# Performance work log

Measured on AMD Instinct MI355X. Metric: run time of the kernel, lower is better.

The kernel has to match this reference:

```python
import jax, jax.numpy as jnp
import numpy as np

B, Q, CTX, H, HKV, D, HID = 2, 1024, 3072, 32, 8, 128, 4096
KV = CTX + Q
EPS = 1e-6


def _rope_tables():
    pos = jnp.arange(KV, dtype=jnp.float32)
    inv_freq = 1.0 / (10000.0 ** (jnp.arange(0, D, 2, dtype=jnp.float32) / D))
    ang = pos[:, None] * inv_freq[None, :]              # [KV, D/2]
    emb = jnp.concatenate([ang, ang], axis=-1)          # [KV, D]
    cos = jnp.broadcast_to(jnp.cos(emb)[None], (B, KV, D))
    sin = jnp.broadcast_to(jnp.sin(emb)[None], (B, KV, D))
    return cos, sin


def setup_inputs() -> dict:
    key = jax.random.key(0)
    ks = jax.random.split(key, 8)
    cos, sin = _rope_tables()
    return {
        "hidden_states": jax.random.normal(ks[0], (B, Q, HID), jnp.float32),
        "context_states": jax.random.normal(ks[1], (B, CTX, HID), jnp.float32),
        "cos": cos,
        "sin": sin,
        "attention_mask": jnp.zeros((B, 1, Q, KV), jnp.float32),
        "Wq": jax.random.normal(ks[2], (HID, H * D), jnp.float32) * 0.02,
        "Wk": jax.random.normal(ks[3], (HID, HKV * D), jnp.float32) * 0.02,
        "Wv": jax.random.normal(ks[4], (HID, HKV * D), jnp.float32) * 0.02,
        "Wo": jax.random.normal(ks[5], (H * D, HID), jnp.float32) * 0.02,
        "q_norm_w": jnp.ones((D,), jnp.float32),
        "k_norm_w": jnp.ones((D,), jnp.float32),
    }


def _rms_norm(x, w):
    var = jnp.mean(x * x, axis=-1, keepdims=True)
    return x * jax.lax.rsqrt(var + EPS) * w


def _rotate_half(x):
    x1, x2 = jnp.split(x, 2, axis=-1)
    return jnp.concatenate([-x2, x1], axis=-1)


def reference(hidden_states, context_states, cos, sin, attention_mask,
              Wq, Wk, Wv, Wo, q_norm_w, k_norm_w):
    # q projection + per-head RMSNorm
    q = (hidden_states @ Wq).reshape(B, Q, H, D)
    q = _rms_norm(q, q_norm_w).transpose(0, 2, 1, 3)      # [B,H,Q,D]
    # k/v: context tokens then noise tokens
    k = jnp.concatenate([context_states @ Wk, hidden_states @ Wk], axis=1)
    k = _rms_norm(k.reshape(B, KV, HKV, D), k_norm_w).transpose(0, 2, 1, 3)  # [B,Hkv,KV,D]
    v = jnp.concatenate([context_states @ Wv, hidden_states @ Wv], axis=1)
    v = v.reshape(B, KV, HKV, D).transpose(0, 2, 1, 3)    # [B,Hkv,KV,D]
    # rotary: q takes the trailing q_len positions of the kv-length tables
    cos4 = cos[:, None, :, :]                             # [B,1,KV,D]
    sin4 = sin[:, None, :, :]
    q = q * cos4[..., -Q:, :] + _rotate_half(q) * sin4[..., -Q:, :]
    k = k * cos4 + _rotate_half(k) * sin4
    # GQA: repeat kv heads to match query heads
    g = H // HKV
    kr = jnp.repeat(k, g, axis=1)                         # [B,H,KV,D]
    vr = jnp.repeat(v, g, axis=1)
    scale = D ** -0.5
    scores = jnp.einsum("bhqd,bhkd->bhqk", q, kr) * scale + attention_mask
    attn = jax.nn.softmax(scores, axis=-1)
    out = jnp.einsum("bhqk,bhkd->bhqd", attn, vr)         # [B,H,Q,D]
    out = out.transpose(0, 2, 1, 3).reshape(B, Q, H * D)
    return out @ Wo
```

## Files before the change

kernel.cpp:

```cpp
#include <hip/hip_runtime.h>
#include <stdint.h>

typedef unsigned short u16;
typedef __attribute__((ext_vector_type(4))) float f32x4;
typedef __attribute__((ext_vector_type(8))) __bf16 bf16x8;
typedef __attribute__((ext_vector_type(2))) __bf16 bf16x2;

#define B_   2
#define Q_   1024
#define CTX_ 3072
#define KV_  4096
#define H_   32
#define HKV_ 8
#define D_   128
#define HID_ 4096

__device__ __forceinline__ u16 f2bf(float f) {
  uint32_t u = __float_as_uint(f);
  u += 0x7fffu + ((u >> 16) & 1u);
  return (u16)(u >> 16);
}
__device__ __forceinline__ float bf2f(u16 h) {
  return __uint_as_float(((uint32_t)h) << 16);
}
__device__ __forceinline__ uint32_t packbf2(float a, float b) {
  return (uint32_t)f2bf(a) | ((uint32_t)f2bf(b) << 16);
}
__device__ __forceinline__ uint32_t pkbf(float a, float b) {
  bf16x2 v = {(__bf16)a, (__bf16)b};
  uint32_t r;
  __builtin_memcpy(&r, &v, 4);
  return r;
}
__device__ __forceinline__ float fexp2(float x) {
#if __has_builtin(__builtin_amdgcn_exp2f)
  return __builtin_amdgcn_exp2f(x);
#else
  return exp2f(x);
#endif
}
__device__ __forceinline__ f32x4 zero4() { f32x4 v = {0.f, 0.f, 0.f, 0.f}; return v; }

__device__ __forceinline__ f32x4 mfma16(bf16x8 a, bf16x8 b, f32x4 c) {
  return __builtin_amdgcn_mfma_f32_16x16x32_bf16(a, b, c, 0, 0, 0);
}

__device__ __forceinline__ void gl2lds16(const void* g, void* l) {
  __builtin_amdgcn_global_load_lds(
      (const __attribute__((address_space(1))) void*)g,
      (__attribute__((address_space(3))) void*)l, 16, 0, 0);
}

__device__ __forceinline__ void bar()    { asm volatile("s_barrier" ::: "memory"); }
__device__ __forceinline__ void waitv8() { asm volatile("s_waitcnt vmcnt(8)" ::: "memory"); }
__device__ __forceinline__ void waitv0() { asm volatile("s_waitcnt vmcnt(0)" ::: "memory"); }

__global__ void conv_bf16(const float* __restrict__ in, u16* __restrict__ out, int n8) {
  int i = blockIdx.x * blockDim.x + threadIdx.x;
  if (i >= n8) return;
  const float4 a = *reinterpret_cast<const float4*>(in + (size_t)i * 8);
  const float4 b = *reinterpret_cast<const float4*>(in + (size_t)i * 8 + 4);
  uint4 o;
  o.x = packbf2(a.x, a.y); o.y = packbf2(a.z, a.w);
  o.z = packbf2(b.x, b.y); o.w = packbf2(b.z, b.w);
  *reinterpret_cast<uint4*>(out + (size_t)i * 8) = o;
}

__global__ void transpose_w(const float* __restrict__ W, u16* __restrict__ WT, int K, int N) {
  __shared__ u16 t[64][68];
  const int n0 = blockIdx.x * 64, k0 = blockIdx.y * 64;
  const int tid = threadIdx.x;
  const int rr = tid >> 4;
  const int cc = (tid & 15) * 4;
#pragma unroll
  for (int p = 0; p < 4; ++p) {
    const int r = p * 16 + rr;
    const float4 v = *reinterpret_cast<const float4*>(W + (size_t)(k0 + r) * N + n0 + cc);
    t[cc + 0][r] = f2bf(v.x);
    t[cc + 1][r] = f2bf(v.y);
    t[cc + 2][r] = f2bf(v.z);
    t[cc + 3][r] = f2bf(v.w);
  }
  __syncthreads();
#pragma unroll
  for (int p = 0; p < 4; ++p) {
    const int n = p * 16 + rr;
    const uint2 w = *reinterpret_cast<const uint2*>(&t[n][cc]);
    *reinterpret_cast<uint2*>(WT + (size_t)(n0 + n) * K + k0 + cc) = w;
  }
}

template <int MODE>
__global__ __launch_bounds__(256, 2) void gemm_bt(
    const u16* __restrict__ A0, const u16* __restrict__ A1,
    const u16* __restrict__ B0, const u16* __restrict__ B1,
    void* __restrict__ Cv, int N) {
  __shared__ u16 lA[2][128 * 64];
  __shared__ u16 lB[2][128 * 64];
  const int tid = threadIdx.x;
  const int lane = tid & 63, wid = tid >> 6;
  const int lq = lane & 15, lg = lane >> 4;
  const int nbn = N >> 7;
  const int bm = (int)blockIdx.x / nbn, bn = (int)blockIdx.x % nbn;
  const int m0 = bm << 7, n0 = bn << 7;
  const int wr = wid >> 1, wc = wid & 1;
  const int sr = lane >> 3;
  const int sc = (lane & 7) << 4;

  f32x4 acc[4][4];
#pragma unroll
  for (int i = 0; i < 4; ++i)
#pragma unroll
    for (int j = 0; j < 4; ++j) acc[i][j] = zero4();

  auto arowp = [&](int m) -> const u16* {
    if constexpr (MODE == 1) {
      const int b = m >> 12, kv = m & 4095;
      return (kv < CTX_) ? (A0 + (size_t)(b * CTX_ + kv) * HID_)
                         : (A1 + (size_t)(b * Q_ + (kv - CTX_)) * HID_);
    } else {
      return A0 + (size_t)m * HID_;
    }
  };
  auto browp = [&](int n) -> const u16* {
    if constexpr (MODE == 1) {
      return (n < 1024) ? (B0 + (size_t)n * HID_) : (B1 + (size_t)(n - 1024) * HID_);
    } else {
      return B0 + (size_t)n * HID_;
    }
  };

  const char* apre[4];
  const char* bpre[4];
#pragma unroll
  for (int j = 0; j < 4; ++j) {
    const int r0 = (wid * 4 + j) * 8;
    const int r = r0 + sr;
    const int sw = sc ^ ((r & 7) << 4);
    apre[j] = (const char*)arowp(m0 + r) + sw;
    bpre[j] = (const char*)browp(n0 + r) + sw;
  }

  auto stage = [&](int cur, int kt) {
    const int kb = kt << 7;
#pragma unroll
    for (int j = 0; j < 4; ++j) {
      const int r0 = (wid * 4 + j) * 8;
      gl2lds16(apre[j] + kb, (char*)&lA[cur][0] + r0 * 128);
      gl2lds16(bpre[j] + kb, (char*)&lB[cur][0] + r0 * 128);
    }
  };

  const int NK = HID_ / 64;
  stage(0, 0);
  stage(1, 1);
  waitv8();
  bar();

  for (int kt = 0; kt < NK; ++kt) {
    const int cur = kt & 1;
    const char* ba = (const char*)&lA[cur][0];
    const char* bb = (const char*)&lB[cur][0];
    bf16x8 af[4][2], bfr[4][2];
#pragma unroll
    for (int mf = 0; mf < 4; ++mf)
#pragma unroll
      for (int kk = 0; kk < 2; ++kk)
        af[mf][kk] = *reinterpret_cast<const bf16x8*>(
            ba + (wr * 64 + mf * 16 + lq) * 128 + ((kk * 64 + lg * 16) ^ ((lq & 7) << 4)));
#pragma unroll
    for (int nf = 0; nf < 4; ++nf)
#pragma unroll
      for (int kk = 0; kk < 2; ++kk)
        bfr[nf][kk] = *reinterpret_cast<const bf16x8*>(
            bb + (wc * 64 + nf * 16 + lq) * 128 + ((kk * 64 + lg * 16) ^ ((lq & 7) << 4)));
    __builtin_amdgcn_s_setprio(1);
#pragma unroll
    for (int mf = 0; mf < 4; ++mf)
#pragma unroll
      for (int nf = 0; nf < 4; ++nf) {
        acc[mf][nf] = mfma16(af[mf][0], bfr[nf][0], acc[mf][nf]);
        acc[mf][nf] = mfma16(af[mf][1], bfr[nf][1], acc[mf][nf]);
      }
    __builtin_amdgcn_s_setprio(0);
    bar();
    if (kt + 2 < NK) {
      stage(cur, kt + 2);
      waitv8();
      bar();
    } else if (kt + 1 < NK) {
      waitv0();
      bar();
    }
  }

#pragma unroll
  for (int mf = 0; mf < 4; ++mf) {
    const int m = m0 + wr * 64 + mf * 16 + lg * 4;
#pragma unroll
    for (int nf = 0; nf < 4; ++nf) {
      const int n = n0 + wc * 64 + nf * 16 + lq;
      if constexpr (MODE == 2) {
        float* C = (float*)Cv;
#pragma unroll
        for (int i = 0; i < 4; ++i) C[(size_t)(m + i) * N + n] = acc[mf][nf][i];
      } else {
        u16* C = (u16*)Cv;
#pragma unroll
        for (int i = 0; i < 4; ++i) C[(size_t)(m + i) * N + n] = f2bf(acc[mf][nf][i]);
      }
    }
  }
}

__global__ void rope_q(const u16* __restrict__ Qp, const float* __restrict__ cosT,
                       const float* __restrict__ sinT, const float* __restrict__ w,
                       u16* __restrict__ Qh) {
  const int row = blockIdx.x * 4 + (threadIdx.x >> 6);
  const int lane = threadIdx.x & 63;
  const int b = row >> 15;
  const int rem = row & 32767;
  const int q = rem >> 5, h = rem & 31;
  const int d = lane * 2;
  const uint32_t raw =
      *reinterpret_cast<const uint32_t*>(Qp + (size_t)(b * Q_ + q) * HID_ + h * D_ + d);
  float x0 = bf2f((u16)(raw & 0xffffu)), x1 = bf2f((u16)(raw >> 16));
  float ss = x0 * x0 + x1 * x1;
#pragma unroll
  for (int m = 1; m < 64; m <<= 1) ss += __shfl_xor(ss, m);
  const float rms = rsqrtf(ss * (1.0f / 128.0f) + 1e-6f);
  const float n0v = x0 * rms * w[d], n1v = x1 * rms * w[d + 1];
  const float p0 = __shfl_xor(n0v, 32), p1 = __shfl_xor(n1v, 32);
  const float r0 = (lane < 32) ? -p0 : p0;
  const float r1 = (lane < 32) ? -p1 : p1;
  const int pos = CTX_ + q;
  const size_t cb = (size_t)(b * KV_ + pos) * D_ + d;
  const float y0 = n0v * cosT[cb] + r0 * sinT[cb];
  const float y1 = n1v * cosT[cb + 1] + r1 * sinT[cb + 1];
  *reinterpret_cast<uint32_t*>(Qh + (size_t)((b * H_ + h) * Q_ + q) * D_ + d) = packbf2(y0, y1);
}

__global__ void rope_k(const u16* __restrict__ KVp, const float* __restrict__ cosT,
                       const float* __restrict__ sinT, const float* __restrict__ w,
                       u16* __restrict__ Kt) {
  const int row = blockIdx.x * 4 + (threadIdx.x >> 6);
  const int lane = threadIdx.x & 63;
  const int b = row >> 15;
  const int rem = row & 32767;
  const int kv = rem >> 3, hk = rem & 7;
  const int d = lane * 2;
  const uint32_t raw =
      *reinterpret_cast<const uint32_t*>(KVp + (size_t)(b * KV_ + kv) * 2048 + hk * D_ + d);
  float x0 = bf2f((u16)(raw & 0xffffu)), x1 = bf2f((u16)(raw >> 16));
  float ss = x0 * x0 + x1 * x1;
#pragma unroll
  for (int m = 1; m < 64; m <<= 1) ss += __shfl_xor(ss, m);
  const float rms = rsqrtf(ss * (1.0f / 128.0f) + 1e-6f);
  const float n0v = x0 * rms * w[d], n1v = x1 * rms * w[d + 1];
  const float p0 = __shfl_xor(n0v, 32), p1 = __shfl_xor(n1v, 32);
  const float r0 = (lane < 32) ? -p0 : p0;
  const float r1 = (lane < 32) ? -p1 : p1;
  const size_t cb = (size_t)(b * KV_ + kv) * D_ + d;
  const float y0 = n0v * cosT[cb] + r0 * sinT[cb];
  const float y1 = n1v * cosT[cb + 1] + r1 * sinT[cb + 1];
  *reinterpret_cast<uint32_t*>(Kt + ((size_t)(b * HKV_ + hk) * KV_ + kv) * D_ + d) =
      packbf2(y0, y1);
}

__global__ void transpose_v(const u16* __restrict__ KVp, u16* __restrict__ Vt) {
  __shared__ u16 t[128][68];
  const int bid = (int)blockIdx.x;
  const int kt = bid & 63;
  const int rest = bid >> 6;
  const int hk = rest & 7, b = rest >> 3;
  const int kv0 = kt * 64;
  const int tid = threadIdx.x;
  const int kvi = tid >> 5;
  const int d4 = (tid & 31) * 4;
#pragma unroll
  for (int p = 0; p < 8; ++p) {
    const int kv = p * 8 + kvi;
    const uint2 v = *reinterpret_cast<const uint2*>(
        KVp + (size_t)(b * KV_ + kv0 + kv) * 2048 + 1024 + hk * D_ + d4);
    t[d4 + 0][kv] = (u16)(v.x & 0xffffu);
    t[d4 + 1][kv] = (u16)(v.x >> 16);
    t[d4 + 2][kv] = (u16)(v.y & 0xffffu);
    t[d4 + 3][kv] = (u16)(v.y >> 16);
  }
  __syncthreads();
  const int dr = tid >> 4;
  const int k4 = (tid & 15) * 4;
#pragma unroll
  for (int p = 0; p < 8; ++p) {
    const int dd = p * 16 + dr;
    const uint2 w = *reinterpret_cast<const uint2*>(&t[dd][k4]);
    *reinterpret_cast<uint2*>(Vt + ((size_t)(b * HKV_ + hk) * D_ + dd) * KV_ + kv0 + k4) = w;
  }
}

__global__ __launch_bounds__(256, 2) void attn(
    const u16* __restrict__ Qh, const u16* __restrict__ Kt,
    const u16* __restrict__ Vt, u16* __restrict__ O) {
  __shared__ u16 lK[2][64 * 128];
  __shared__ u16 lV[2][128 * 64];
  __shared__ u16 lP[4][2][16 * 64];
  const int bid0 = (int)blockIdx.x;
  const int lb = (bid0 & 7) * 64 + (bid0 >> 3);
  const int qt = lb & 7;
  const int rest = lb >> 3;
  const int g4 = rest & 3;
  const int bhk = rest >> 2;
  const int b = bhk >> 3, hk = bhk & 7;
  const int h = hk * 4 + g4;
  const int tid = threadIdx.x;
  const int lane = tid & 63, wid = tid >> 6;
  const int lq = lane & 15, lg = lane >> 4;
  const int q0 = qt * 128 + wid * 32;

  const char* qrow = (const char*)(Qh + ((size_t)(b * H_ + h) * Q_ + q0 + lq) * D_);
  bf16x8 qf[2][4];
#pragma unroll
  for (int kk = 0; kk < 4; ++kk) {
    qf[0][kk] = *reinterpret_cast<const bf16x8*>(qrow + kk * 64 + lg * 16);
    qf[1][kk] = *reinterpret_cast<const bf16x8*>(qrow + 16 * 256 + kk * 64 + lg * 16);
  }

  const char* KtB = (const char*)(Kt + (size_t)(b * HKV_ + hk) * KV_ * D_);
  const char* VtB = (const char*)(Vt + (size_t)(b * HKV_ + hk) * D_ * KV_);

  f32x4 oac[2][8];
#pragma unroll
  for (int qb = 0; qb < 2; ++qb)
#pragma unroll
    for (int i = 0; i < 8; ++i) oac[qb][i] = zero4();
  float mrow[2] = {-1e30f, -1e30f}, lsum[2] = {0.f, 0.f};

  const int kr = lane >> 4;
  const int kcb = (lane & 15) << 4;
  const int vr = lane >> 3;
  const int vcb = (lane & 7) << 4;

  const char* kpre[4];
  const char* vpre[4];
#pragma unroll
  for (int j = 0; j < 4; ++j) {
    const int krow = (wid * 4 + j) * 4 + kr;
    kpre[j] = KtB + (size_t)krow * 256 + (kcb ^ ((krow & 7) << 4));
    const int dd = (wid * 4 + j) * 8 + vr;
    vpre[j] = VtB + (size_t)dd * (KV_ * 2) + (vcb ^ ((dd & 7) << 4));
  }

  auto stage = [&](int cur, int t) {
    const size_t kv0 = (size_t)(t << 6);
#pragma unroll
    for (int j = 0; j < 4; ++j) {
      const int r0 = (wid * 4 + j) * 4;
      gl2lds16(kpre[j] + kv0 * 256, (char*)&lK[cur][0] + r0 * 256);
    }
#pragma unroll
    for (int j = 0; j < 4; ++j) {
      const int d0 = (wid * 4 + j) * 8;
      gl2lds16(vpre[j] + kv0 * 2, (char*)&lV[cur][0] + d0 * 128);
    }
  };

  const int NT = KV_ / 64;
  stage(0, 0);
  stage(1, 1);
  waitv8();
  bar();

  const float c1 = 0.12752134f;
  char* pb0 = (char*)&lP[wid][0][0];
  char* pb1 = (char*)&lP[wid][1][0];
  for (int t = 0; t < NT; ++t) {
    const int cur = t & 1;
    const char* kb = (const char*)&lK[cur][0];
    const char* vb = (const char*)&lV[cur][0];
    f32x4 sa[2][4];
    __builtin_amdgcn_s_setprio(1);
#pragma unroll
    for (int h16 = 0; h16 < 4; ++h16) {
      const int row = h16 * 16 + lq;
      bf16x8 kf[4];
#pragma unroll
      for (int kk = 0; kk < 4; ++kk)
        kf[kk] = *reinterpret_cast<const bf16x8*>(
            kb + row * 256 + ((kk * 64 + lg * 16) ^ ((lq & 7) << 4)));
      f32x4 s0 = zero4(), s1 = zero4();
#pragma unroll
      for (int kk = 0; kk < 4; ++kk) {
        s0 = mfma16(kf[kk], qf[0][kk], s0);
        s1 = mfma16(kf[kk], qf[1][kk], s1);
      }
      sa[0][h16] = s0;
      sa[1][h16] = s1;
    }
    __builtin_amdgcn_s_setprio(0);
#pragma unroll
    for (int qb = 0; qb < 2; ++qb) {
      const f32x4 s0v = sa[qb][0], s1v = sa[qb][1], s2v = sa[qb][2], s3v = sa[qb][3];
      float ta = fmaxf(fmaxf(s0v[0], s0v[1]), s0v[2]);
      float tb = fmaxf(fmaxf(s0v[3], s1v[0]), s1v[1]);
      float tc = fmaxf(fmaxf(s1v[2], s1v[3]), s2v[0]);
      float td = fmaxf(fmaxf(s2v[1], s2v[2]), s2v[3]);
      float te = fmaxf(fmaxf(s3v[0], s3v[1]), s3v[2]);
      float tmax = fmaxf(fmaxf(fmaxf(ta, tb), tc), fmaxf(fmaxf(td, te), s3v[3]));
      tmax = fmaxf(tmax, __shfl_xor(tmax, 16));
      tmax = fmaxf(tmax, __shfl_xor(tmax, 32));
      float p[4][4];
      if (!__all((tmax - mrow[qb]) * c1 <= 3.0f)) {
        const float mnew = fmaxf(mrow[qb], tmax);
        const float resc = fexp2((mrow[qb] - mnew) * c1);
        mrow[qb] = mnew;
        lsum[qb] *= resc;
#pragma unroll
        for (int i = 0; i < 8; ++i) oac[qb][i] *= resc;
      }
      const float mc = mrow[qb] * c1;
#pragma unroll
      for (int h16 = 0; h16 < 4; ++h16)
#pragma unroll
        for (int i = 0; i < 4; ++i)
          p[h16][i] = fexp2(fmaf(sa[qb][h16][i], c1, -mc));
      float q01 = (p[0][0] + p[0][1]) + (p[0][2] + p[0][3]);
      float q23 = (p[1][0] + p[1][1]) + (p[1][2] + p[1][3]);
      float q45 = (p[2][0] + p[2][1]) + (p[2][2] + p[2][3]);
      float q67 = (p[3][0] + p[3][1]) + (p[3][2] + p[3][3]);
      lsum[qb] += (q01 + q23) + (q45 + q67);
      char* pb = qb ? pb1 : pb0;
#pragma unroll
      for (int h16 = 0; h16 < 4; ++h16) {
        uint2 pw;
        pw.x = pkbf(p[h16][0], p[h16][1]);
        pw.y = pkbf(p[h16][2], p[h16][3]);
        *reinterpret_cast<uint2*>(pb + lq * 128 + ((h16 * 32 + lg * 8) ^ ((lq & 7) << 4))) = pw;
      }
    }
    asm volatile("" ::: "memory");
    __builtin_amdgcn_s_setprio(1);
#pragma unroll
    for (int c = 0; c < 2; ++c) {
      const int po = lq * 128 + ((lg * 16 + c * 64) ^ ((lq & 7) << 4));
      const bf16x8 pf0 = *reinterpret_cast<const bf16x8*>(pb0 + po);
      const bf16x8 pf1 = *reinterpret_cast<const bf16x8*>(pb1 + po);
#pragma unroll
      for (int db = 0; db < 8; ++db) {
        const int dd = db * 16 + lq;
        const bf16x8 vf = *reinterpret_cast<const bf16x8*>(
            vb + dd * 128 + ((lg * 16 + c * 64) ^ ((dd & 7) << 4)));
        oac[0][db] = mfma16(vf, pf0, oac[0][db]);
        oac[1][db] = mfma16(vf, pf1, oac[1][db]);
      }
    }
    __builtin_amdgcn_s_setprio(0);
    bar();
    if (t + 2 < NT) {
      stage(cur, t + 2);
      waitv8();
      bar();
    } else if (t + 1 < NT) {
      waitv0();
      bar();
    }
  }
#pragma unroll
  for (int qb = 0; qb < 2; ++qb) {
    float lt = lsum[qb] + __shfl_xor(lsum[qb], 16);
    lt += __shfl_xor(lt, 32);
    const float inv = 1.0f / lt;
    u16* orow = O + (size_t)(b * Q_ + q0 + qb * 16 + lq) * (H_ * D_) + h * D_;
#pragma unroll
    for (int db = 0; db < 8; ++db) {
      uint2 wv;
      wv.x = pkbf(oac[qb][db][0] * inv, oac[qb][db][1] * inv);
      wv.y = pkbf(oac[qb][db][2] * inv, oac[qb][db][3] * inv);
      *reinterpret_cast<uint2*>((char*)orow + db * 32 + lg * 8) = wv;
    }
  }
}

extern "C" void kernel_launch(void* const* d_in, const int* in_sizes, int n_in,
                              void* d_out, int out_size, void* d_ws, size_t ws_size,
                              hipStream_t stream) {
  (void)in_sizes; (void)n_in; (void)out_size; (void)ws_size;
  const float* hidden  = (const float*)d_in[0];
  const float* context = (const float*)d_in[1];
  const float* cosT    = (const float*)d_in[2];
  const float* sinT    = (const float*)d_in[3];
  const float* Wq = (const float*)d_in[5];
  const float* Wk = (const float*)d_in[6];
  const float* Wv = (const float*)d_in[7];
  const float* Wo = (const float*)d_in[8];
  const float* qw = (const float*)d_in[9];
  const float* kw = (const float*)d_in[10];

  char* ws = (char*)d_ws;
  u16* hidB = (u16*)(ws + 0);
  u16* ctxB = (u16*)(ws + 16777216);
  u16* WqT  = (u16*)(ws + 67108864);
  u16* WkT  = (u16*)(ws + 100663296);
  u16* WvT  = (u16*)(ws + 109051904);
  u16* WoT  = (u16*)(ws + 117440512);
  u16* Qp   = (u16*)(ws + 150994944);
  u16* KVp  = (u16*)(ws + 167772160);
  u16* Qh   = (u16*)(ws + 201326592);
  u16* Kt   = (u16*)(ws + 218103808);
  u16* Vt   = (u16*)(ws + 234881024);
  u16* Obuf = hidB;

  conv_bf16<<<4096, 256, 0, stream>>>(hidden, hidB, 1048576);
  conv_bf16<<<12288, 256, 0, stream>>>(context, ctxB, 3145728);
  transpose_w<<<dim3(64, 64), 256, 0, stream>>>(Wq, WqT, 4096, 4096);
  transpose_w<<<dim3(16, 64), 256, 0, stream>>>(Wk, WkT, 4096, 1024);
  transpose_w<<<dim3(16, 64), 256, 0, stream>>>(Wv, WvT, 4096, 1024);
  transpose_w<<<dim3(64, 64), 256, 0, stream>>>(Wo, WoT, 4096, 4096);
  gemm_bt<0><<<512, 256, 0, stream>>>(hidB, nullptr, WqT, nullptr, Qp, 4096);
  gemm_bt<1><<<1024, 256, 0, stream>>>(ctxB, hidB, WkT, WvT, KVp, 2048);
  rope_q<<<16384, 256, 0, stream>>>(Qp, cosT, sinT, qw, Qh);
  rope_k<<<16384, 256, 0, stream>>>(KVp, cosT, sinT, kw, Kt);
  transpose_v<<<1024, 256, 0, stream>>>(KVp, Vt);
  attn<<<512, 256, 0, stream>>>(Qh, Kt, Vt, Obuf);
  gemm_bt<2><<<512, 256, 0, stream>>>(Obuf, nullptr, WoT, nullptr, d_out, 4096);
}
```

Measured before the change: 618.1 us.

## Use dedicated 256x256-tile 8-wave GEMM for fused K/V projection

Replaces the 128x128-tile generic GEMM for the K/V projection with a new kernel that uses 256x256 tiles, 512 threads and a split-K-half staging schedule. Loads are interleaved with MFMA phases, wave priority is raised around the MFMA blocks, and the block index is remapped to group tiles for L2 reuse. The aim is more operand reuse per byte loaded and better overlap of global-to-LDS traffic with compute. The cost is higher register pressure from the 8x4 accumulators and more barriers per K step. The generic GEMM drops its unused dual-pointer mode.

```diff
diff --git a/kernel.cpp b/kernel.cpp
--- a/kernel.cpp
+++ b/kernel.cpp
@@ -53,6 +53,7 @@
 
 __device__ __forceinline__ void bar()    { asm volatile("s_barrier" ::: "memory"); }
 __device__ __forceinline__ void waitv8() { asm volatile("s_waitcnt vmcnt(8)" ::: "memory"); }
+__device__ __forceinline__ void waitv4() { asm volatile("s_waitcnt vmcnt(4)" ::: "memory"); }
 __device__ __forceinline__ void waitv0() { asm volatile("s_waitcnt vmcnt(0)" ::: "memory"); }
 
 __global__ void conv_bf16(const float* __restrict__ in, u16* __restrict__ out, int n8) {
@@ -92,8 +93,7 @@
 
 template <int MODE>
 __global__ __launch_bounds__(256, 2) void gemm_bt(
-    const u16* __restrict__ A0, const u16* __restrict__ A1,
-    const u16* __restrict__ B0, const u16* __restrict__ B1,
+    const u16* __restrict__ A0, const u16* __restrict__ B0,
     void* __restrict__ Cv, int N) {
   __shared__ u16 lA[2][128 * 64];
   __shared__ u16 lB[2][128 * 64];
@@ -113,23 +113,6 @@
 #pragma unroll
     for (int j = 0; j < 4; ++j) acc[i][j] = zero4();
 
-  auto arowp = [&](int m) -> const u16* {
-    if constexpr (MODE == 1) {
-      const int b = m >> 12, kv = m & 4095;
-      return (kv < CTX_) ? (A0 + (size_t)(b * CTX_ + kv) * HID_)
-                         : (A1 + (size_t)(b * Q_ + (kv - CTX_)) * HID_);
-    } else {
-      return A0 + (size_t)m * HID_;
-    }
-  };
-  auto browp = [&](int n) -> const u16* {
-    if constexpr (MODE == 1) {
-      return (n < 1024) ? (B0 + (size_t)n * HID_) : (B1 + (size_t)(n - 1024) * HID_);
-    } else {
-      return B0 + (size_t)n * HID_;
-    }
-  };
-
   const char* apre[4];
   const char* bpre[4];
 #pragma unroll
@@ -137,8 +120,8 @@
     const int r0 = (wid * 4 + j) * 8;
     const int r = r0 + sr;
     const int sw = sc ^ ((r & 7) << 4);
-    apre[j] = (const char*)arowp(m0 + r) + sw;
-    bpre[j] = (const char*)browp(n0 + r) + sw;
+    apre[j] = (const char*)(A0 + (size_t)(m0 + r) * HID_) + sw;
+    bpre[j] = (const char*)(B0 + (size_t)(n0 + r) * HID_) + sw;
   }
 
   auto stage = [&](int cur, int kt) {
@@ -209,6 +192,142 @@
 #pragma unroll
         for (int i = 0; i < 4; ++i) C[(size_t)(m + i) * N + n] = f2bf(acc[mf][nf][i]);
       }
+    }
+  }
+}
+
+__global__ __launch_bounds__(512, 2) void gemm_kv8(
+    const u16* __restrict__ A0, const u16* __restrict__ A1,
+    const u16* __restrict__ B0, const u16* __restrict__ B1,
+    u16* __restrict__ C) {
+  __shared__ u16 lA[2][2][256 * 32];
+  __shared__ u16 lB[2][2][256 * 32];
+  const int tid = threadIdx.x;
+  const int lane = tid & 63, wid = tid >> 6;
+  const int lq = lane & 15, lg = lane >> 4;
+  const int lb = ((int)blockIdx.x & 7) * 32 + ((int)blockIdx.x >> 3);
+  const int bm = lb >> 3, bn = lb & 7;
+  const int m0 = bm << 8, n0 = bn << 8;
+  const int wr = wid >> 2, wc = wid & 3;
+
+  f32x4 acc[8][4];
+#pragma unroll
+  for (int i = 0; i < 8; ++i)
+#pragma unroll
+    for (int j = 0; j < 4; ++j) acc[i][j] = zero4();
+
+  auto arowp = [&](int m) -> const u16* {
+    const int b = m >> 12, kv = m & 4095;
+    return (kv < CTX_) ? (A0 + (size_t)(b * CTX_ + kv) * HID_)
+                       : (A1 + (size_t)(b * Q_ + (kv - CTX_)) * HID_);
+  };
+  auto browp = [&](int n) -> const u16* {
+    return (n < 1024) ? (B0 + (size_t)n * HID_) : (B1 + (size_t)(n - 1024) * HID_);
+  };
+
+  const char* apre[2];
+  const char* bpre[2];
+  int ldst[2];
+#pragma unroll
+  for (int j = 0; j < 2; ++j) {
+    const int rr = wid * 32 + j * 16 + (lane >> 2);
+    const int ch = ((lane & 3) ^ ((rr >> 1) & 3)) << 4;
+    apre[j] = (const char*)arowp(m0 + rr) + ch;
+    bpre[j] = (const char*)browp(n0 + rr) + ch;
+    ldst[j] = (wid * 32 + j * 16) * 64;
+  }
+
+  auto stageA = [&](int buf, int kh, int t) {
+    const int kb = (t << 7) + (kh << 6);
+#pragma unroll
+    for (int j = 0; j < 2; ++j)
+      gl2lds16(apre[j] + kb, (char*)&lA[buf][kh][0] + ldst[j]);
+  };
+  auto stageB = [&](int buf, int kh, int t) {
+    const int kb = (t << 7) + (kh << 6);
+#pragma unroll
+    for (int j = 0; j < 2; ++j)
+      gl2lds16(bpre[j] + kb, (char*)&lB[buf][kh][0] + ldst[j]);
+  };
+
+  auto rdA = [&](int buf, int kh, int mf) -> bf16x8 {
+    const int row = wr * 128 + mf * 16 + lq;
+    return *reinterpret_cast<const bf16x8*>(
+        (const char*)&lA[buf][kh][0] + row * 64 + ((lg * 16) ^ (((row >> 1) & 3) << 4)));
+  };
+  auto rdB = [&](int buf, int kh, int nf) -> bf16x8 {
+    const int row = wc * 64 + nf * 16 + lq;
+    return *reinterpret_cast<const bf16x8*>(
+        (const char*)&lB[buf][kh][0] + row * 64 + ((lg * 16) ^ (((row >> 1) & 3) << 4)));
+  };
+
+  const int NK = HID_ / 64;
+  stageA(0, 0, 0); stageB(0, 0, 0); stageA(0, 1, 0); stageB(0, 1, 0);
+
+  bf16x8 af[4], bfr[4];
+  for (int t = 0; t < NK; ++t) {
+    const int buf = t & 1, nb = buf ^ 1;
+    const bool pf = (t + 1 < NK);
+    waitv4();
+    if (pf) stageA(nb, 0, t + 1);
+    bar();
+#pragma unroll
+    for (int mf = 0; mf < 4; ++mf) af[mf] = rdA(buf, 0, mf);
+#pragma unroll
+    for (int nf = 0; nf < 4; ++nf) bfr[nf] = rdB(buf, 0, nf);
+    __builtin_amdgcn_s_setprio(1);
+#pragma unroll
+    for (int mf = 0; mf < 4; ++mf)
+#pragma unroll
+      for (int nf = 0; nf < 4; ++nf) acc[mf][nf] = mfma16(af[mf], bfr[nf], acc[mf][nf]);
+    __builtin_amdgcn_s_setprio(0);
+    bar();
+    if (pf) stageB(nb, 0, t + 1);
+    bar();
+#pragma unroll
+    for (int mf = 0; mf < 4; ++mf) af[mf] = rdA(buf, 0, mf + 4);
+    __builtin_amdgcn_s_setprio(1);
+#pragma unroll
+    for (int mf = 0; mf < 4; ++mf)
+#pragma unroll
+      for (int nf = 0; nf < 4; ++nf) acc[mf + 4][nf] = mfma16(af[mf], bfr[nf], acc[mf + 4][nf]);
+    __builtin_amdgcn_s_setprio(0);
+    bar();
+    if (pf) { waitv4(); stageA(nb, 1, t + 1); }
+    else    { waitv0(); }
+    bar();
+#pragma unroll
+    for (int mf = 0; mf < 4; ++mf) af[mf] = rdA(buf, 1, mf);
+#pragma unroll
+    for (int nf = 0; nf < 4; ++nf) bfr[nf] = rdB(buf, 1, nf);
+    __builtin_amdgcn_s_setprio(1);
+#pragma unroll
+    for (int mf = 0; mf < 4; ++mf)
+#pragma unroll
+      for (int nf = 0; nf < 4; ++nf) acc[mf][nf] = mfma16(af[mf], bfr[nf], acc[mf][nf]);
+    __builtin_amdgcn_s_setprio(0);
+    bar();
+    if (pf) stageB(nb, 1, t + 1);
+    bar();
+#pragma unroll
+    for (int mf = 0; mf < 4; ++mf) af[mf] = rdA(buf, 1, mf + 4);
+    __builtin_amdgcn_s_setprio(1);
+#pragma unroll
+    for (int mf = 0; mf < 4; ++mf)
+#pragma unroll
+      for (int nf = 0; nf < 4; ++nf) acc[mf + 4][nf] = mfma16(af[mf], bfr[nf], acc[mf + 4][nf]);
+    __builtin_amdgcn_s_setprio(0);
+    bar();
+  }
+
+#pragma unroll
+  for (int mf = 0; mf < 8; ++mf) {
+    const int m = m0 + wr * 128 + mf * 16 + lg * 4;
+#pragma unroll
+    for (int nf = 0; nf < 4; ++nf) {
+      const int n = n0 + wc * 64 + nf * 16 + lq;
+#pragma unroll
+      for (int i = 0; i < 4; ++i) C[(size_t)(m + i) * 2048 + n] = f2bf(acc[mf][nf][i]);
     }
   }
 }
@@ -515,11 +634,11 @@
   transpose_w<<<dim3(16, 64), 256, 0, stream>>>(Wk, WkT, 4096, 1024);
   transpose_w<<<dim3(16, 64), 256, 0, stream>>>(Wv, WvT, 4096, 1024);
   transpose_w<<<dim3(64, 64), 256, 0, stream>>>(Wo, WoT, 4096, 4096);
-  gemm_bt<0><<<512, 256, 0, stream>>>(hidB, nullptr, WqT, nullptr, Qp, 4096);
-  gemm_bt<1><<<1024, 256, 0, stream>>>(ctxB, hidB, WkT, WvT, KVp, 2048);
+  gemm_bt<0><<<512, 256, 0, stream>>>(hidB, WqT, Qp, 4096);
+  gemm_kv8<<<256, 512, 0, stream>>>(ctxB, hidB, WkT, WvT, KVp);
   rope_q<<<16384, 256, 0, stream>>>(Qp, cosT, sinT, qw, Qh);
   rope_k<<<16384, 256, 0, stream>>>(KVp, cosT, sinT, kw, Kt);
   transpose_v<<<1024, 256, 0, stream>>>(KVp, Vt);
   attn<<<512, 256, 0, stream>>>(Qh, Kt, Vt, Obuf);
-  gemm_bt<2><<<512, 256, 0, stream>>>(Obuf, nullptr, WoT, nullptr, d_out, 4096);
-}
+  gemm_bt<2><<<512, 256, 0, stream>>>(Obuf, WoT, d_out, 4096);
+}
```

New measurement: 623.9 us. No clear change (+0.9%).

## Fuse RMSNorm+RoPE and V transpose into projection GEMM epilogues

Applied to the files above, without the earlier changes.

The Q and K/V projection GEMMs now stage their fp32 accumulators in shared memory and apply per-head RMSNorm and rotary embedding (or transpose V) directly in the epilogue. This removes three separate elementwise/transpose kernels and the intermediate Qp/KVp round trip through global memory. LDS offsets in the GEMM and attention loops are also precomputed once into registers. Shared memory grows to 128x129 floats per block (about 66 KB), which may lower occupancy. The epilogue also adds a serial per-thread pass over 64 elements with cos/sin loads.

```diff
diff --git a/kernel.cpp b/kernel.cpp
--- a/kernel.cpp
+++ b/kernel.cpp
@@ -91,12 +91,15 @@
 }
 
 template <int MODE>
-__global__ __launch_bounds__(256, 2) void gemm_bt(
+__global__ __launch_bounds__(256, 2) void gemm_fused(
     const u16* __restrict__ A0, const u16* __restrict__ A1,
     const u16* __restrict__ B0, const u16* __restrict__ B1,
-    void* __restrict__ Cv, int N) {
-  __shared__ u16 lA[2][128 * 64];
-  __shared__ u16 lB[2][128 * 64];
+    const float* __restrict__ cosT, const float* __restrict__ sinT,
+    const float* __restrict__ nw,
+    void* __restrict__ out0, void* __restrict__ out1, int N) {
+  __shared__ float scr[128 * 129];
+  u16* lA = (u16*)scr;
+  u16* lB = lA + 2 * 128 * 64;
   const int tid = threadIdx.x;
   const int lane = tid & 63, wid = tid >> 6;
   const int lq = lane & 15, lg = lane >> 4;
@@ -141,13 +144,22 @@
     bpre[j] = (const char*)browp(n0 + r) + sw;
   }
 
+  int aoff[4][2], boff[4][2];
+#pragma unroll
+  for (int mf = 0; mf < 4; ++mf)
+#pragma unroll
+    for (int kk = 0; kk < 2; ++kk) {
+      aoff[mf][kk] = (wr * 64 + mf * 16 + lq) * 128 + ((kk * 64 + lg * 16) ^ ((lq & 7) << 4));
+      boff[mf][kk] = (wc * 64 + mf * 16 + lq) * 128 + ((kk * 64 + lg * 16) ^ ((lq & 7) << 4));
+    }
+
   auto stage = [&](int cur, int kt) {
     const int kb = kt << 7;
 #pragma unroll
     for (int j = 0; j < 4; ++j) {
       const int r0 = (wid * 4 + j) * 8;
-      gl2lds16(apre[j] + kb, (char*)&lA[cur][0] + r0 * 128);
-      gl2lds16(bpre[j] + kb, (char*)&lB[cur][0] + r0 * 128);
+      gl2lds16(apre[j] + kb, (char*)lA + cur * 16384 + r0 * 128);
+      gl2lds16(bpre[j] + kb, (char*)lB + cur * 16384 + r0 * 128);
     }
   };
 
@@ -159,21 +171,19 @@
 
   for (int kt = 0; kt < NK; ++kt) {
     const int cur = kt & 1;
-    const char* ba = (const char*)&lA[cur][0];
-    const char* bb = (const char*)&lB[cur][0];
+    const char* ba = (const char*)lA + cur * 16384;
+    const char* bb = (const char*)lB + cur * 16384;
     bf16x8 af[4][2], bfr[4][2];
 #pragma unroll
     for (int mf = 0; mf < 4; ++mf)
 #pragma unroll
       for (int kk = 0; kk < 2; ++kk)
-        af[mf][kk] = *reinterpret_cast<const bf16x8*>(
-            ba + (wr * 64 + mf * 16 + lq) * 128 + ((kk * 64 + lg * 16) ^ ((lq & 7) << 4)));
+        af[mf][kk] = *reinterpret_cast<const bf16x8*>(ba + aoff[mf][kk]);
 #pragma unroll
     for (int nf = 0; nf < 4; ++nf)
 #pragma unroll
       for (int kk = 0; kk < 2; ++kk)
-        bfr[nf][kk] = *reinterpret_cast<const bf16x8*>(
-            bb + (wc * 64 + nf * 16 + lq) * 128 + ((kk * 64 + lg * 16) ^ ((lq & 7) << 4)));
+        bfr[nf][kk] = *reinterpret_cast<const bf16x8*>(bb + boff[nf][kk]);
     __builtin_amdgcn_s_setprio(1);
 #pragma unroll
     for (int mf = 0; mf < 4; ++mf)
@@ -194,107 +204,96 @@
     }
   }
 
-#pragma unroll
-  for (int mf = 0; mf < 4; ++mf) {
-    const int m = m0 + wr * 64 + mf * 16 + lg * 4;
-#pragma unroll
-    for (int nf = 0; nf < 4; ++nf) {
-      const int n = n0 + wc * 64 + nf * 16 + lq;
-      if constexpr (MODE == 2) {
-        float* C = (float*)Cv;
+  if constexpr (MODE == 2) {
+    float* C = (float*)out0;
+#pragma unroll
+    for (int mf = 0; mf < 4; ++mf) {
+      const int m = m0 + wr * 64 + mf * 16 + lg * 4;
+#pragma unroll
+      for (int nf = 0; nf < 4; ++nf) {
+        const int n = n0 + wc * 64 + nf * 16 + lq;
 #pragma unroll
         for (int i = 0; i < 4; ++i) C[(size_t)(m + i) * N + n] = acc[mf][nf][i];
-      } else {
-        u16* C = (u16*)Cv;
-#pragma unroll
-        for (int i = 0; i < 4; ++i) C[(size_t)(m + i) * N + n] = f2bf(acc[mf][nf][i]);
-      }
-    }
-  }
-}
-
-__global__ void rope_q(const u16* __restrict__ Qp, const float* __restrict__ cosT,
-                       const float* __restrict__ sinT, const float* __restrict__ w,
-                       u16* __restrict__ Qh) {
-  const int row = blockIdx.x * 4 + (threadIdx.x >> 6);
-  const int lane = threadIdx.x & 63;
-  const int b = row >> 15;
-  const int rem = row & 32767;
-  const int q = rem >> 5, h = rem & 31;
-  const int d = lane * 2;
-  const uint32_t raw =
-      *reinterpret_cast<const uint32_t*>(Qp + (size_t)(b * Q_ + q) * HID_ + h * D_ + d);
-  float x0 = bf2f((u16)(raw & 0xffffu)), x1 = bf2f((u16)(raw >> 16));
-  float ss = x0 * x0 + x1 * x1;
-#pragma unroll
-  for (int m = 1; m < 64; m <<= 1) ss += __shfl_xor(ss, m);
-  const float rms = rsqrtf(ss * (1.0f / 128.0f) + 1e-6f);
-  const float n0v = x0 * rms * w[d], n1v = x1 * rms * w[d + 1];
-  const float p0 = __shfl_xor(n0v, 32), p1 = __shfl_xor(n1v, 32);
-  const float r0 = (lane < 32) ? -p0 : p0;
-  const float r1 = (lane < 32) ? -p1 : p1;
-  const int pos = CTX_ + q;
-  const size_t cb = (size_t)(b * KV_ + pos) * D_ + d;
-  const float y0 = n0v * cosT[cb] + r0 * sinT[cb];
-  const float y1 = n1v * cosT[cb + 1] + r1 * sinT[cb + 1];
-  *reinterpret_cast<uint32_t*>(Qh + (size_t)((b * H_ + h) * Q_ + q) * D_ + d) = packbf2(y0, y1);
-}
-
-__global__ void rope_k(const u16* __restrict__ KVp, const float* __restrict__ cosT,
-                       const float* __restrict__ sinT, const float* __restrict__ w,
-                       u16* __restrict__ Kt) {
-  const int row = blockIdx.x * 4 + (threadIdx.x >> 6);
-  const int lane = threadIdx.x & 63;
-  const int b = row >> 15;
-  const int rem = row & 32767;
-  const int kv = rem >> 3, hk = rem & 7;
-  const int d = lane * 2;
-  const uint32_t raw =
-      *reinterpret_cast<const uint32_t*>(KVp + (size_t)(b * KV_ + kv) * 2048 + hk * D_ + d);
-  float x0 = bf2f((u16)(raw & 0xffffu)), x1 = bf2f((u16)(raw >> 16));
-  float ss = x0 * x0 + x1 * x1;
-#pragma unroll
-  for (int m = 1; m < 64; m <<= 1) ss += __shfl_xor(ss, m);
-  const float rms = rsqrtf(ss * (1.0f / 128.0f) + 1e-6f);
-  const float n0v = x0 * rms * w[d], n1v = x1 * rms * w[d + 1];
-  const float p0 = __shfl_xor(n0v, 32), p1 = __shfl_xor(n1v, 32);
-  const float r0 = (lane < 32) ? -p0 : p0;
-  const float r1 = (lane < 32) ? -p1 : p1;
-  const size_t cb = (size_t)(b * KV_ + kv) * D_ + d;
-  const float y0 = n0v * cosT[cb] + r0 * sinT[cb];
-  const float y1 = n1v * cosT[cb + 1] + r1 * sinT[cb + 1];
-  *reinterpret_cast<uint32_t*>(Kt + ((size_t)(b * HKV_ + hk) * KV_ + kv) * D_ + d) =
-      packbf2(y0, y1);
-}
-
-__global__ void transpose_v(const u16* __restrict__ KVp, u16* __restrict__ Vt) {
-  __shared__ u16 t[128][68];
-  const int bid = (int)blockIdx.x;
-  const int kt = bid & 63;
-  const int rest = bid >> 6;
-  const int hk = rest & 7, b = rest >> 3;
-  const int kv0 = kt * 64;
-  const int tid = threadIdx.x;
-  const int kvi = tid >> 5;
-  const int d4 = (tid & 31) * 4;
-#pragma unroll
-  for (int p = 0; p < 8; ++p) {
-    const int kv = p * 8 + kvi;
-    const uint2 v = *reinterpret_cast<const uint2*>(
-        KVp + (size_t)(b * KV_ + kv0 + kv) * 2048 + 1024 + hk * D_ + d4);
-    t[d4 + 0][kv] = (u16)(v.x & 0xffffu);
-    t[d4 + 1][kv] = (u16)(v.x >> 16);
-    t[d4 + 2][kv] = (u16)(v.y & 0xffffu);
-    t[d4 + 3][kv] = (u16)(v.y >> 16);
-  }
-  __syncthreads();
-  const int dr = tid >> 4;
-  const int k4 = (tid & 15) * 4;
-#pragma unroll
-  for (int p = 0; p < 8; ++p) {
-    const int dd = p * 16 + dr;
-    const uint2 w = *reinterpret_cast<const uint2*>(&t[dd][k4]);
-    *reinterpret_cast<uint2*>(Vt + ((size_t)(b * HKV_ + hk) * D_ + dd) * KV_ + kv0 + k4) = w;
+      }
+    }
+    return;
+  }
+
+#pragma unroll
+  for (int mf = 0; mf < 4; ++mf)
+#pragma unroll
+    for (int nf = 0; nf < 4; ++nf)
+#pragma unroll
+      for (int i = 0; i < 4; ++i)
+        scr[(wr * 64 + mf * 16 + lg * 4 + i) * 129 + wc * 64 + nf * 16 + lq] = acc[mf][nf][i];
+  bar();
+
+  const bool isK = (MODE == 0) || (bn < 8);
+  if (isK) {
+    const int r = tid >> 1, half = tid & 1;
+    int bb, pos;
+    u16* orow;
+    if constexpr (MODE == 0) {
+      bb = m0 >> 10;
+      const int q = (m0 & 1023) + r;
+      pos = CTX_ + q;
+      orow = (u16*)out0 + ((size_t)(bb * H_ + bn) * Q_ + q) * D_ + half * 64;
+    } else {
+      bb = m0 >> 12;
+      pos = (m0 & 4095) + r;
+      orow = (u16*)out0 + ((size_t)(bb * HKV_ + (bn & 7)) * KV_ + pos) * D_ + half * 64;
+    }
+    const float* base  = &scr[r * 129 + half * 64];
+    const float* pbase = &scr[r * 129 + (half ^ 1) * 64];
+    f32x4 xv[16];
+    float ss = 0.f;
+#pragma unroll
+    for (int j = 0; j < 16; ++j) {
+      xv[j] = *reinterpret_cast<const f32x4*>(base + 4 * j);
+      ss += xv[j][0] * xv[j][0] + xv[j][1] * xv[j][1] +
+            xv[j][2] * xv[j][2] + xv[j][3] * xv[j][3];
+    }
+    ss += __shfl_xor(ss, 1);
+    const float rms = rsqrtf(ss * (1.0f / 128.0f) + 1e-6f);
+    const float sgn = half ? 1.f : -1.f;
+    const float* cp  = cosT + (size_t)(bb * KV_ + pos) * D_ + half * 64;
+    const float* sp  = sinT + (size_t)(bb * KV_ + pos) * D_ + half * 64;
+    const float* wpo = nw + half * 64;
+    const float* wpp = nw + (half ^ 1) * 64;
+#pragma unroll
+    for (int j = 0; j < 16; j += 2) {
+      uint4 o;
+#pragma unroll
+      for (int u = 0; u < 2; ++u) {
+        const f32x4 pv = *reinterpret_cast<const f32x4*>(pbase + 4 * (j + u));
+        const f32x4 cv = *reinterpret_cast<const f32x4*>(cp + 4 * (j + u));
+        const f32x4 sv = *reinterpret_cast<const f32x4*>(sp + 4 * (j + u));
+        const f32x4 wo = *reinterpret_cast<const f32x4*>(wpo + 4 * (j + u));
+        const f32x4 wp = *reinterpret_cast<const f32x4*>(wpp + 4 * (j + u));
+        float y[4];
+#pragma unroll
+        for (int e = 0; e < 4; ++e)
+          y[e] = (xv[j + u][e] * rms * wo[e]) * cv[e] + sgn * (pv[e] * rms * wp[e]) * sv[e];
+        (&o.x)[u * 2 + 0] = pkbf(y[0], y[1]);
+        (&o.x)[u * 2 + 1] = pkbf(y[2], y[3]);
+      }
+      *reinterpret_cast<uint4*>((char*)orow + (j >> 1) * 16) = o;
+    }
+  } else {
+    const int bb = m0 >> 12, kv0 = m0 & 4095;
+    const int dloc = tid >> 1, kh = tid & 1;
+    u16* orow = (u16*)out1 + ((size_t)(bb * HKV_ + (bn & 7)) * D_ + dloc) * KV_ + kv0 + kh * 64;
+#pragma unroll
+    for (int j = 0; j < 8; ++j) {
+      uint4 o;
+#pragma unroll
+      for (int e = 0; e < 4; ++e) {
+        const float a = scr[(kh * 64 + j * 8 + 2 * e) * 129 + dloc];
+        const float c = scr[(kh * 64 + j * 8 + 2 * e + 1) * 129 + dloc];
+        (&o.x)[e] = pkbf(a, c);
+      }
+      *reinterpret_cast<uint4*>((char*)orow + j * 16) = o;
+    }
   }
 }
 
@@ -350,6 +349,27 @@
     vpre[j] = VtB + (size_t)dd * (KV_ * 2) + (vcb ^ ((dd & 7) << 4));
   }
 
+  int koff[4][4];
+#pragma unroll
+  for (int h16 = 0; h16 < 4; ++h16)
+#pragma unroll
+    for (int kk = 0; kk < 4; ++kk)
+      koff[h16][kk] = (h16 * 16 + lq) * 256 + ((kk * 64 + lg * 16) ^ ((lq & 7) << 4));
+  int voff[2][8];
+#pragma unroll
+  for (int c = 0; c < 2; ++c)
+#pragma unroll
+    for (int db = 0; db < 8; ++db)
+      voff[c][db] = (db * 16 + lq) * 128 + ((lg * 16 + c * 64) ^ ((lq & 7) << 4));
+  int poffw[4];
+#pragma unroll
+  for (int h16 = 0; h16 < 4; ++h16)
+    poffw[h16] = lq * 128 + ((h16 * 32 + lg * 8) ^ ((lq & 7) << 4));
+  int poffr[2];
+#pragma unroll
+  for (int c = 0; c < 2; ++c)
+    poffr[c] = lq * 128 + ((lg * 16 + c * 64) ^ ((lq & 7) << 4));
+
   auto stage = [&](int cur, int t) {
     const size_t kv0 = (size_t)(t << 6);
 #pragma unroll
@@ -381,12 +401,10 @@
     __builtin_amdgcn_s_setprio(1);
 #pragma unroll
     for (int h16 = 0; h16 < 4; ++h16) {
-      const int row = h16 * 16 + lq;
       bf16x8 kf[4];
 #pragma unroll
       for (int kk = 0; kk < 4; ++kk)
-        kf[kk] = *reinterpret_cast<const bf16x8*>(
-            kb + row * 256 + ((kk * 64 + lg * 16) ^ ((lq & 7) << 4)));
+        kf[kk] = *reinterpret_cast<const bf16x8*>(kb + koff[h16][kk]);
       f32x4 s0 = zero4(), s1 = zero4();
 #pragma unroll
       for (int kk = 0; kk < 4; ++kk) {
@@ -434,21 +452,18 @@
         uint2 pw;
         pw.x = pkbf(p[h16][0], p[h16][1]);
         pw.y = pkbf(p[h16][2], p[h16][3]);
-        *reinterpret_cast<uint2*>(pb + lq * 128 + ((h16 * 32 + lg * 8) ^ ((lq & 7) << 4))) = pw;
+        *reinterpret_cast<uint2*>(pb + poffw[h16]) = pw;
       }
     }
     asm volatile("" ::: "memory");
     __builtin_amdgcn_s_setprio(1);
 #pragma unroll
     for (int c = 0; c < 2; ++c) {
-      const int po = lq * 128 + ((lg * 16 + c * 64) ^ ((lq & 7) << 4));
-      const bf16x8 pf0 = *reinterpret_cast<const bf16x8*>(pb0 + po);
-      const bf16x8 pf1 = *reinterpret_cast<const bf16x8*>(pb1 + po);
+      const bf16x8 pf0 = *reinterpret_cast<const bf16x8*>(pb0 + poffr[c]);
+      const bf16x8 pf1 = *reinterpret_cast<const bf16x8*>(pb1 + poffr[c]);
 #pragma unroll
       for (int db = 0; db < 8; ++db) {
-        const int dd = db * 16 + lq;
-        const bf16x8 vf = *reinterpret_cast<const bf16x8*>(
-            vb + dd * 128 + ((lg * 16 + c * 64) ^ ((dd & 7) << 4)));
+        const bf16x8 vf = *reinterpret_cast<const bf16x8*>(vb + voff[c][db]);
         oac[0][db] = mfma16(vf, pf0, oac[0][db]);
         oac[1][db] = mfma16(vf, pf1, oac[1][db]);
       }
@@ -502,8 +517,6 @@
   u16* WkT  = (u16*)(ws + 100663296);
   u16* WvT  = (u16*)(ws + 109051904);
   u16* WoT  = (u16*)(ws + 117440512);
-  u16* Qp   = (u16*)(ws + 150994944);
-  u16* KVp  = (u16*)(ws + 167772160);
   u16* Qh   = (u16*)(ws + 201326592);
   u16* Kt   = (u16*)(ws + 218103808);
   u16* Vt   = (u16*)(ws + 234881024);
@@ -515,11 +528,11 @@
   transpose_w<<<dim3(16, 64), 256, 0, stream>>>(Wk, WkT, 4096, 1024);
   transpose_w<<<dim3(16, 64), 256, 0, stream>>>(Wv, WvT, 4096, 1024);
   transpose_w<<<dim3(64, 64), 256, 0, stream>>>(Wo, WoT, 4096, 4096);
-  gemm_bt<0><<<512, 256, 0, stream>>>(hidB, nullptr, WqT, nullptr, Qp, 4096);
-  gemm_bt<1><<<1024, 256, 0, stream>>>(ctxB, hidB, WkT, WvT, KVp, 2048);
-  rope_q<<<16384, 256, 0, stream>>>(Qp, cosT, sinT, qw, Qh);
-  rope_k<<<16384, 256, 0, stream>>>(KVp, cosT, sinT, kw, Kt);
-  transpose_v<<<1024, 256, 0, stream>>>(KVp, Vt);
+  gemm_fused<0><<<512, 256, 0, stream>>>(hidB, nullptr, WqT, nullptr,
+                                         cosT, sinT, qw, Qh, nullptr, 4096);
+  gemm_fused<1><<<1024, 256, 0, stream>>>(ctxB, hidB, WkT, WvT,
+                                          cosT, sinT, kw, Kt, Vt, 2048);
   attn<<<512, 256, 0, stream>>>(Qh, Kt, Vt, Obuf);
-  gemm_bt<2><<<512, 256, 0, stream>>>(Obuf, nullptr, WoT, nullptr, d_out, 4096);
-}
+  gemm_fused<2><<<512, 256, 0, stream>>>(Obuf, nullptr, WoT, nullptr,
+                                         nullptr, nullptr, nullptr, d_out, nullptr, 4096);
+}
```

Measured after the change: 569.8 us. 7.8% less time.
